# Kernel optimization log

Hardware: AMD Instinct MI355X
Metric: run time of the kernel (lower is better)

## Reference

```python
import jax, jax.numpy as jnp
import numpy as np

EPS = 1e-12  # matches torch F.normalize default eps


def setup_inputs() -> dict:
    key = jax.random.key(0)
    k1, k2 = jax.random.split(key)
    B, S, H, E = 4, 4096, 4096, 64
    hidden_states = jax.random.normal(k1, (B, S, H), dtype=jnp.float32)
    sim_matrix = jax.random.normal(k2, (H, E), dtype=jnp.float32)
    gates = jnp.zeros((E,), dtype=jnp.float32)
    return {"hidden_states": hidden_states, "sim_matrix": sim_matrix, "gates": gates}


def _l2_normalize(x, axis):
    # torch F.normalize: x / max(||x||, eps)
    n = jnp.linalg.norm(x, axis=axis, keepdims=True)
    return x / jnp.maximum(n, EPS)


def reference(hidden_states, sim_matrix, gates):
    norm_h = _l2_normalize(hidden_states, axis=-1)          # [B,S,H]
    norm_w = _l2_normalize(sim_matrix, axis=0)               # [H,E]
    raw_logits = jnp.einsum('bsh,he->bse', norm_h, norm_w)   # [B,S,E]
    scaled_logits = jax.nn.sigmoid(raw_logits)
    scaled_gates = jax.nn.sigmoid(gates)                     # [E]
    activated_scores = jax.nn.relu(scaled_logits - scaled_gates)
    return (raw_logits, scaled_logits, activated_scores)
```

## Files before the change

### kernel.cpp

```cpp
#include <hip/hip_runtime.h>
#include <hip/hip_bf16.h>

typedef __bf16 bf16x8 __attribute__((ext_vector_type(8)));
typedef float f32x4 __attribute__((ext_vector_type(4)));

#define HDIM 4096
#define EDIM 64
#define KBLK 128
#define NW 8
#define KBW (KBLK/NW)
#define NRG 4

__global__ __launch_bounds__(256) void pack_w_kernel(const float* __restrict__ W,
                                                     __bf16* __restrict__ Wp,
                                                     float* __restrict__ partial) {
  const int b = blockIdx.x;
  const int t = threadIdx.x;
  const int e = t & 63;
  const int nt = e >> 4, col = e & 15;
  __shared__ float red[256];
  float s = 0.f;
  const int base = b * 64 * 64;
#pragma unroll
  for (int i = 0; i < 16; ++i) {
    int flat = base + i * 256 + t;
    float v = W[flat];
    s = fmaf(v, v, s);
    int r = flat >> 6;
    int kb = r >> 5, g = (r >> 3) & 3, j = r & 7;
    Wp[(size_t)((nt * KBLK + kb) * 64 + col + 16 * g) * 8 + j] = (__bf16)v;
  }
  red[t] = s;
  __syncthreads();
  if (t < 64)
    partial[b * 64 + t] = red[t] + red[t + 64] + red[t + 128] + red[t + 192];
}

__global__ __launch_bounds__(512, 1) void gate_main_kernel(
    const float* __restrict__ H, const __bf16* __restrict__ Wp,
    const float* __restrict__ G, const float* __restrict__ partial,
    float* __restrict__ out, size_t third) {
  const int lane = threadIdx.x & 63;
  const int w = threadIdx.x >> 6;
  const int m = lane & 15;
  const int g = lane >> 4;
  const int row0 = blockIdx.x * 64;

  __shared__ float lds_acc[NRG][4][4][NW][64];
  __shared__ float lds_ssq[NW][64];
  __shared__ float lds_invw[64];

  if (threadIdx.x < 64) {
    float cs = 0.f;
#pragma unroll 8
    for (int i = 0; i < 64; ++i) cs += partial[i * 64 + threadIdx.x];
    lds_invw[threadIdx.x] = 1.0f / fmaxf(sqrtf(cs), 1e-12f);
  }

  const int kb0 = w * KBW;
  const float* hp0 = H + (size_t)(row0 + 0 * 16 + m) * HDIM + kb0 * 32 + g * 8;
  const float* hp1 = hp0 + (size_t)16 * HDIM;
  const float* hp2 = hp0 + (size_t)32 * HDIM;
  const float* hp3 = hp0 + (size_t)48 * HDIM;
  const bf16x8* bbase = reinterpret_cast<const bf16x8*>(Wp) + lane;

  f32x4 acc[NRG][4] = {};
  float ssqa[NRG], ssqb[NRG];
#pragma unroll
  for (int rg = 0; rg < NRG; ++rg) { ssqa[rg] = 0.f; ssqb[rg] = 0.f; }

#pragma unroll 2
  for (int i = 0; i < KBW; ++i) {
    float4 a0[NRG], a1[NRG];
    a0[0] = *(const float4*)(hp0 + (size_t)i * 32);
    a1[0] = *(const float4*)(hp0 + (size_t)i * 32 + 4);
    a0[1] = *(const float4*)(hp1 + (size_t)i * 32);
    a1[1] = *(const float4*)(hp1 + (size_t)i * 32 + 4);
    a0[2] = *(const float4*)(hp2 + (size_t)i * 32);
    a1[2] = *(const float4*)(hp2 + (size_t)i * 32 + 4);
    a0[3] = *(const float4*)(hp3 + (size_t)i * 32);
    a1[3] = *(const float4*)(hp3 + (size_t)i * 32 + 4);

    bf16x8 bfr[4];
#pragma unroll
    for (int nt = 0; nt < 4; ++nt)
      bfr[nt] = bbase[(size_t)(nt * KBLK + kb0 + i) * 64];

#pragma unroll
    for (int rg = 0; rg < NRG; ++rg) {
      bf16x8 af;
      af[0] = (__bf16)a0[rg].x; af[1] = (__bf16)a0[rg].y;
      af[2] = (__bf16)a0[rg].z; af[3] = (__bf16)a0[rg].w;
      af[4] = (__bf16)a1[rg].x; af[5] = (__bf16)a1[rg].y;
      af[6] = (__bf16)a1[rg].z; af[7] = (__bf16)a1[rg].w;

      ssqa[rg] = fmaf(a0[rg].x, a0[rg].x, ssqa[rg]);
      ssqb[rg] = fmaf(a0[rg].y, a0[rg].y, ssqb[rg]);
      ssqa[rg] = fmaf(a0[rg].z, a0[rg].z, ssqa[rg]);
      ssqb[rg] = fmaf(a0[rg].w, a0[rg].w, ssqb[rg]);
      ssqa[rg] = fmaf(a1[rg].x, a1[rg].x, ssqa[rg]);
      ssqb[rg] = fmaf(a1[rg].y, a1[rg].y, ssqb[rg]);
      ssqa[rg] = fmaf(a1[rg].z, a1[rg].z, ssqa[rg]);
      ssqb[rg] = fmaf(a1[rg].w, a1[rg].w, ssqb[rg]);

#pragma unroll
      for (int nt = 0; nt < 4; ++nt)
        acc[rg][nt] = __builtin_amdgcn_mfma_f32_16x16x32_bf16(af, bfr[nt], acc[rg][nt], 0, 0, 0);
    }
  }

#pragma unroll
  for (int rg = 0; rg < NRG; ++rg) {
    float ssq = ssqa[rg] + ssqb[rg];
    ssq += __shfl_xor(ssq, 16, 64);
    ssq += __shfl_xor(ssq, 32, 64);
    if (g == 0) lds_ssq[w][rg * 16 + m] = ssq;
#pragma unroll
    for (int nt = 0; nt < 4; ++nt)
#pragma unroll
      for (int r = 0; r < 4; ++r)
        lds_acc[rg][nt][r][w][lane] = acc[rg][nt][r];
  }
  __syncthreads();

  {
    const int e = lane;
    const float invw = lds_invw[e];
    const float sg = 1.0f / (1.0f + __expf(-G[e]));
    const int nt = e >> 4;
#pragma unroll
    for (int rr = 0; rr < 8; ++rr) {
      const int R = w * 8 + rr;
      const int rg = R >> 4;
      const int r = R & 3;
      const int lsrc = (((R >> 2) & 3) << 4) | (e & 15);
      float st = 0.f, a = 0.f;
#pragma unroll
      for (int s = 0; s < NW; ++s) {
        st += lds_ssq[s][R];
        a += lds_acc[rg][nt][r][s][lsrc];
      }
      float invh = 1.0f / fmaxf(sqrtf(st), 1e-12f);
      float raw = a * invh * invw;
      float sig = 1.0f / (1.0f + __expf(-raw));
      size_t idx = (size_t)(row0 + R) * EDIM + e;
      out[idx] = raw;
      out[idx + third] = sig;
      out[idx + 2 * third] = fmaxf(sig - sg, 0.0f);
    }
  }
}

extern "C" void kernel_launch(void* const* d_in, const int* in_sizes, int n_in,
                              void* d_out, int out_size, void* d_ws, size_t ws_size,
                              hipStream_t stream) {
  const float* H = (const float*)d_in[0];
  const float* W = (const float*)d_in[1];
  const float* G = (const float*)d_in[2];
  float* out = (float*)d_out;
  __bf16* Wp = (__bf16*)d_ws;
  float* partial = (float*)((char*)d_ws + 512 * 1024);

  int rows = in_sizes[0] / HDIM;
  size_t third = (size_t)out_size / 3;

  pack_w_kernel<<<64, 256, 0, stream>>>(W, Wp, partial);
  gate_main_kernel<<<rows / 64, 512, 0, stream>>>(H, Wp, G, partial, out, third);
}
```

Measured before the change: 57.71 us.

## Stage hidden-state tiles through LDS with async global_load_lds double buffering

Replaces direct per-lane float4 global loads of H with coalesced 16-byte global_load_lds transfers into a per-wave double-buffered, XOR-swizzled LDS region. Explicit vmcnt waits let the next K-block stream in while the current one is converted to bf16 and fed to MFMA. The same LDS buffer is reused for the cross-wave accumulator reduction. This adds an LDS round trip, a sync before reuse, and relies on hand-counted vmcnt values being correct.

```diff
diff --git a/kernel.cpp b/kernel.cpp
--- a/kernel.cpp
+++ b/kernel.cpp
@@ -3,6 +3,7 @@
 
 typedef __bf16 bf16x8 __attribute__((ext_vector_type(8)));
 typedef float f32x4 __attribute__((ext_vector_type(4)));
+typedef unsigned int u32;
 
 #define HDIM 4096
 #define EDIM 64
@@ -36,6 +37,12 @@
     partial[b * 64 + t] = red[t] + red[t + 64] + red[t + 128] + red[t + 192];
 }
 
+__device__ __forceinline__ void gload16(const float* g, char* l) {
+  __builtin_amdgcn_global_load_lds(
+      (const __attribute__((address_space(1))) u32*)g,
+      (__attribute__((address_space(3))) u32*)l, 16, 0, 0);
+}
+
 __global__ __launch_bounds__(512, 1) void gate_main_kernel(
     const float* __restrict__ H, const __bf16* __restrict__ Wp,
     const float* __restrict__ G, const float* __restrict__ partial,
@@ -46,7 +53,7 @@
   const int g = lane >> 4;
   const int row0 = blockIdx.x * 64;
 
-  __shared__ float lds_acc[NRG][4][4][NW][64];
+  __shared__ __align__(16) char smem[NW * 16 * 1024];
   __shared__ float lds_ssq[NW][64];
   __shared__ float lds_invw[64];
 
@@ -56,12 +63,19 @@
     for (int i = 0; i < 64; ++i) cs += partial[i * 64 + threadIdx.x];
     lds_invw[threadIdx.x] = 1.0f / fmaxf(sqrtf(cs), 1e-12f);
   }
+  __syncthreads();
 
   const int kb0 = w * KBW;
-  const float* hp0 = H + (size_t)(row0 + 0 * 16 + m) * HDIM + kb0 * 32 + g * 8;
-  const float* hp1 = hp0 + (size_t)16 * HDIM;
-  const float* hp2 = hp0 + (size_t)32 * HDIM;
-  const float* hp3 = hp0 + (size_t)48 * HDIM;
+  char* sb = smem + w * 16384;
+
+  const int lr = lane >> 3;
+  const int lc = (lane & 7) ^ lr;
+  const float* hbase = H + (size_t)(row0 + lr) * HDIM + kb0 * 32 + lc * 4;
+
+  const int sw = (m & 7) << 4;
+  const int rb0 = m * 128 + ((g * 32) ^ sw);
+  const int rb1 = m * 128 + ((g * 32 + 16) ^ sw);
+
   const bf16x8* bbase = reinterpret_cast<const bf16x8*>(Wp) + lane;
 
   f32x4 acc[NRG][4] = {};
@@ -69,45 +83,54 @@
 #pragma unroll
   for (int rg = 0; rg < NRG; ++rg) { ssqa[rg] = 0.f; ssqb[rg] = 0.f; }
 
-#pragma unroll 2
+#define STAGE(buf, I) { _Pragma("unroll")                                      \
+    for (int c = 0; c < 8; ++c)                                                \
+      gload16(hbase + (size_t)c * 8 * HDIM + (size_t)(I) * 32, (buf) + c * 1024); }
+
+  STAGE(sb, 0);
+
   for (int i = 0; i < KBW; ++i) {
-    float4 a0[NRG], a1[NRG];
-    a0[0] = *(const float4*)(hp0 + (size_t)i * 32);
-    a1[0] = *(const float4*)(hp0 + (size_t)i * 32 + 4);
-    a0[1] = *(const float4*)(hp1 + (size_t)i * 32);
-    a1[1] = *(const float4*)(hp1 + (size_t)i * 32 + 4);
-    a0[2] = *(const float4*)(hp2 + (size_t)i * 32);
-    a1[2] = *(const float4*)(hp2 + (size_t)i * 32 + 4);
-    a0[3] = *(const float4*)(hp3 + (size_t)i * 32);
-    a1[3] = *(const float4*)(hp3 + (size_t)i * 32 + 4);
+    char* cur = sb + (i & 1) * 8192;
+    if (i + 1 < KBW) STAGE(sb + ((i + 1) & 1) * 8192, i + 1);
 
     bf16x8 bfr[4];
 #pragma unroll
     for (int nt = 0; nt < 4; ++nt)
       bfr[nt] = bbase[(size_t)(nt * KBLK + kb0 + i) * 64];
 
+    if (i + 1 < KBW) asm volatile("s_waitcnt vmcnt(12)" ::: "memory");
+    else             asm volatile("s_waitcnt vmcnt(4)" ::: "memory");
+    __builtin_amdgcn_sched_barrier(0);
+
 #pragma unroll
     for (int rg = 0; rg < NRG; ++rg) {
+      f32x4 x0 = *(const f32x4*)(cur + rg * 2048 + rb0);
+      f32x4 x1 = *(const f32x4*)(cur + rg * 2048 + rb1);
+
       bf16x8 af;
-      af[0] = (__bf16)a0[rg].x; af[1] = (__bf16)a0[rg].y;
-      af[2] = (__bf16)a0[rg].z; af[3] = (__bf16)a0[rg].w;
-      af[4] = (__bf16)a1[rg].x; af[5] = (__bf16)a1[rg].y;
-      af[6] = (__bf16)a1[rg].z; af[7] = (__bf16)a1[rg].w;
+      af[0] = (__bf16)x0[0]; af[1] = (__bf16)x0[1];
+      af[2] = (__bf16)x0[2]; af[3] = (__bf16)x0[3];
+      af[4] = (__bf16)x1[0]; af[5] = (__bf16)x1[1];
+      af[6] = (__bf16)x1[2]; af[7] = (__bf16)x1[3];
 
-      ssqa[rg] = fmaf(a0[rg].x, a0[rg].x, ssqa[rg]);
-      ssqb[rg] = fmaf(a0[rg].y, a0[rg].y, ssqb[rg]);
-      ssqa[rg] = fmaf(a0[rg].z, a0[rg].z, ssqa[rg]);
-      ssqb[rg] = fmaf(a0[rg].w, a0[rg].w, ssqb[rg]);
-      ssqa[rg] = fmaf(a1[rg].x, a1[rg].x, ssqa[rg]);
-      ssqb[rg] = fmaf(a1[rg].y, a1[rg].y, ssqb[rg]);
-      ssqa[rg] = fmaf(a1[rg].z, a1[rg].z, ssqa[rg]);
-      ssqb[rg] = fmaf(a1[rg].w, a1[rg].w, ssqb[rg]);
+      ssqa[rg] = fmaf(x0[0], x0[0], ssqa[rg]);
+      ssqb[rg] = fmaf(x0[1], x0[1], ssqb[rg]);
+      ssqa[rg] = fmaf(x0[2], x0[2], ssqa[rg]);
+      ssqb[rg] = fmaf(x0[3], x0[3], ssqb[rg]);
+      ssqa[rg] = fmaf(x1[0], x1[0], ssqa[rg]);
+      ssqb[rg] = fmaf(x1[1], x1[1], ssqb[rg]);
+      ssqa[rg] = fmaf(x1[2], x1[2], ssqa[rg]);
+      ssqb[rg] = fmaf(x1[3], x1[3], ssqb[rg]);
 
 #pragma unroll
       for (int nt = 0; nt < 4; ++nt)
         acc[rg][nt] = __builtin_amdgcn_mfma_f32_16x16x32_bf16(af, bfr[nt], acc[rg][nt], 0, 0, 0);
     }
   }
+#undef STAGE
+
+  __syncthreads();
+  float (*lds_acc)[4][4][NW][64] = (float (*)[4][4][NW][64])smem;
 
 #pragma unroll
   for (int rg = 0; rg < NRG; ++rg) {
```

Measured after the change: 57.88 us. About the same (+0.3%).
